# Optimization experiments

Hardware: AMD Instinct MI355X
Metric: run time of the kernel (lower is better)

## Reference

```python
import jax, jax.numpy as jnp
import numpy as np

R, TOTAL, N_NODE, B = 4, 32768, 1024, 32
D_IN, D_HID, C, H, NCLS = 256, 256, 8, 8, 10
E = 262144


def setup_inputs() -> dict:
    key = jax.random.key(0)
    ks = jax.random.split(key, 20)
    s = 0.05  # weight scale for numerical stability
    return {
        "h": jax.random.normal(ks[0], (TOTAL, D_IN), jnp.float32),
        "src": jax.random.randint(ks[1], (R, E), 0, TOTAL),
        "dst": jax.random.randint(ks[2], (R, E), 0, TOTAL),
        "node_label": jax.random.randint(ks[3], (TOTAL,), 0, C),
        "feat_label": jax.random.randint(ks[4], (D_HID,), 0, C),
        "W1": jax.random.normal(ks[5], (R, D_IN, D_HID), jnp.float32) * s,
        "b1": jnp.zeros((R, D_HID), jnp.float32),
        "W2": jax.random.normal(ks[6], (R, D_HID, D_HID), jnp.float32) * s,
        "b2": jnp.zeros((R, D_HID), jnp.float32),
        "Wr": jax.random.normal(ks[7], (C, D_HID, D_HID), jnp.float32) * s,
        "br": jnp.zeros((C, D_HID), jnp.float32),
        "Wq": jax.random.normal(ks[8], (D_HID, D_HID), jnp.float32) * s,
        "Wk": jax.random.normal(ks[9], (D_HID, D_HID), jnp.float32) * s,
        "Wv": jax.random.normal(ks[10], (D_HID, D_HID), jnp.float32) * s,
        "lin_w": jax.random.normal(ks[11], (D_HID, D_HID), jnp.float32) * s,
        "lin_b": jnp.zeros((D_HID,), jnp.float32),
        "bn_gamma": jnp.ones((D_HID,), jnp.float32),
        "bn_beta": jnp.zeros((D_HID,), jnp.float32),
        "cls_w": jax.random.normal(ks[12], (NCLS, D_HID), jnp.float32) * s,
        "cls_b": jnp.zeros((NCLS,), jnp.float32),
    }


def _gconv(x, src, dst, W, b, n):
    # DGL GraphConv norm='both' with self-loops added (dgl.add_self_loop)
    loop = jnp.arange(n)
    s = jnp.concatenate([src, loop])
    d = jnp.concatenate([dst, loop])
    ones = jnp.ones(s.shape, jnp.float32)
    deg_out = jnp.maximum(jax.ops.segment_sum(ones, s, num_segments=n), 1.0)
    deg_in = jnp.maximum(jax.ops.segment_sum(ones, d, num_segments=n), 1.0)
    msg = x[s] * jax.lax.rsqrt(deg_out)[s][:, None]          # [E+n, D]
    agg = jax.ops.segment_sum(msg, d, num_segments=n)        # [n, D]
    agg = agg * jax.lax.rsqrt(deg_in)[:, None]
    return agg @ W + b


def _hetero_layer(x, src, dst, W, b, n):
    # HeteroGraphConv: per-relation GraphConv, 'sum' cross-relation aggregation
    out = 0.0
    for r in range(R):
        out = out + _gconv(x, src[r], dst[r], W[r], b[r], n)
    return out


def _attention(x, Wq, Wk, Wv, lin_w, lin_b):
    # FeatureAttentionLayer (eval mode: no attn dropout)
    b, c, d = x.shape
    dh = d // H
    q = (x @ Wq).reshape(b, c, H, dh).transpose(2, 0, 1, 3)   # [H,B,C,dh]
    k = (x @ Wk).reshape(b, c, H, dh).transpose(2, 0, 1, 3)
    v = (x @ Wv).reshape(b, c, H, dh).transpose(2, 0, 1, 3)
    scores = jnp.einsum('hbqd,hbkd->hbqk', q, k) / jnp.sqrt(jnp.float32(c))
    attn = jax.nn.softmax(scores, axis=-1)
    o = jnp.einsum('hbqk,hbkd->hbqd', attn, v)
    o = o.transpose(1, 2, 0, 3).reshape(b, c, d)              # [B,C,D]
    ff = jax.nn.relu(o @ lin_w.T + lin_b) + o                 # feedforward + inner residual
    out = ff + x                                              # outer residual
    return jnp.mean(out, axis=1)                              # [B,D]


def reference(h, src, dst, node_label, feat_label, W1, b1, W2, b2, Wr, br,
              Wq, Wk, Wv, lin_w, lin_b, bn_gamma, bn_beta, cls_w, cls_b):
    n = h.shape[0]
    # RGCN: conv1 -> relu -> conv2
    h1 = jax.nn.relu(_hetero_layer(h, src, dst, W1, b1, n))
    h2 = _hetero_layer(h1, src, dst, W2, b2, n)               # [TOTAL, D_HID]

    node_emb = h2.reshape(B, N_NODE, D_HID)
    node_mask0 = node_label.reshape(B, N_NODE)[0]             # first graph's node types

    # cluster-wise masked pooling + per-cluster linear resize
    pooled = []
    for key in range(C):
        fmask = (feat_label == key).astype(h2.dtype)          # [D]
        nmask = (node_mask0 == key).astype(h2.dtype)          # [N]
        cnt = jnp.maximum(nmask.sum(), 1.0)
        v = jnp.einsum('bnd,n->bd', node_emb, nmask) / cnt    # mean over cluster's nodes
        v = v * fmask[None, :]                                # keep only cluster's features
        pooled.append(v @ Wr[key].T + br[key])
    emb_in = jnp.stack(pooled, axis=1)                        # [B, C, D]

    graph_emb = _attention(emb_in, Wq, Wk, Wv, lin_w, lin_b)  # [B, D]

    hg_raw = jnp.mean(node_emb, axis=1)                       # dgl.mean_nodes per graph
    diff = graph_emb.reshape(-1) - hg_raw.reshape(-1)
    recon = jnp.sqrt(jnp.sum(jnp.square(diff + 1e-6)))        # pairwise_distance p=2

    # BatchNorm1d with batch statistics, dropout identity (eval)
    mu = jnp.mean(graph_emb, axis=0)
    var = jnp.var(graph_emb, axis=0)
    hg = (graph_emb - mu) * jax.lax.rsqrt(var + 1e-5) * bn_gamma + bn_beta
    logits = hg @ cls_w.T + cls_b                             # [B, NCLS]
    return logits, recon
```

## Files before the change

kernel.cpp:

```cpp
#include <hip/hip_runtime.h>
#include <math.h>

#define R_ 4
#define TOTAL_ 32768
#define NNODE_ 1024
#define B_ 32
#define DH_ 256
#define C_ 8
#define H_ 8
#define NCLS_ 10
#define E_ 262144
#define S_ 32
#define CHUNK_ (E_ / S_)

typedef __attribute__((ext_vector_type(4))) float f32x4;
typedef __attribute__((ext_vector_type(2))) float f32x2;
typedef __attribute__((ext_vector_type(2))) unsigned int uint2v;
typedef __attribute__((ext_vector_type(4))) unsigned int uint4v;
typedef long long i64;

__device__ inline unsigned short f2bf(float f) {
  unsigned int u = __builtin_bit_cast(unsigned int, f);
  u += 0x7FFF + ((u >> 16) & 1);
  return (unsigned short)(u >> 16);
}
__device__ inline float bf2f(unsigned short s) {
  return __builtin_bit_cast(float, (unsigned int)s << 16);
}


__global__ __launch_bounds__(1024) void hist_part(const int* __restrict__ src,
                                                  const int* __restrict__ dst,
                                                  unsigned int* __restrict__ parts) {
  int r = blockIdx.y, s = blockIdx.x, t = threadIdx.x;
  __shared__ unsigned int hs[16384], hd[16384];
  for (int i = t; i < 16384; i += 1024) { hs[i] = 0; hd[i] = 0; }
  __syncthreads();
  const int* sp = src + (size_t)r * E_ + s * CHUNK_;
  const int* dp = dst + (size_t)r * E_ + s * CHUNK_;
  for (int i = t; i < CHUNK_; i += 1024) {
    int a = sp[i], b = dp[i];
    atomicAdd(&hs[a >> 1], 1u << ((a & 1) * 16));
    atomicAdd(&hd[b >> 1], 1u << ((b & 1) * 16));
  }
  __syncthreads();
  unsigned int* po = parts + ((size_t)(r * S_ + s) * 2) * 16384;
  for (int i = t; i < 16384; i += 1024) { po[i] = hs[i]; po[16384 + i] = hd[i]; }
}

__global__ void reduce_deg(const unsigned int* __restrict__ parts,
                           float* __restrict__ rs_out, float* __restrict__ rs_in,
                           int* __restrict__ cnt_in) {
  int gid = blockIdx.x * 256 + threadIdx.x;
  int r = gid >> 14, w = gid & 16383;
  unsigned int s0 = 0, s1 = 0, d0 = 0, d1 = 0;
  for (int s = 0; s < S_; s++) {
    unsigned int ws_ = parts[((size_t)(r * S_ + s) * 2) * 16384 + w];
    unsigned int wd  = parts[((size_t)(r * S_ + s) * 2 + 1) * 16384 + w];
    s0 += ws_ & 0xffff; s1 += ws_ >> 16;
    d0 += wd & 0xffff;  d1 += wd >> 16;
  }
  int n0 = w * 2, n1 = n0 + 1;
  rs_out[r * TOTAL_ + n0] = rsqrtf((float)(s0 + 1));
  rs_out[r * TOTAL_ + n1] = rsqrtf((float)(s1 + 1));
  rs_in[r * TOTAL_ + n0]  = rsqrtf((float)(d0 + 1));
  rs_in[r * TOTAL_ + n1]  = rsqrtf((float)(d1 + 1));
  cnt_in[r * TOTAL_ + n0] = (int)d0;
  cnt_in[r * TOTAL_ + n1] = (int)d1;
}

__global__ __launch_bounds__(1024) void scan_counts(const int* __restrict__ cnt_in,
                                                    int* __restrict__ off) {
  int r = blockIdx.x;
  const int* c = cnt_in + r * TOTAL_;
  int* o = off + r * (TOTAL_ + 1);
  __shared__ int part[1024];
  int t = threadIdx.x;
  int base = t * 32;
  int loc[32];
  int s = 0;
#pragma unroll
  for (int j = 0; j < 32; j++) { loc[j] = c[base + j]; s += loc[j]; }
  part[t] = s;
  __syncthreads();
  for (int d = 1; d < 1024; d <<= 1) {
    int v = (t >= d) ? part[t - d] : 0;
    __syncthreads();
    part[t] += v;
    __syncthreads();
  }
  int run = (t == 0) ? 0 : part[t - 1];
#pragma unroll
  for (int j = 0; j < 32; j++) {
    o[base + j] = run;
    run += loc[j];
  }
  if (t == 1023) o[TOTAL_] = run;
}

__global__ void base_gen(const unsigned int* __restrict__ parts,
                         const int* __restrict__ csr_off,
                         unsigned int* __restrict__ sbb) {
  int gid = blockIdx.x * 256 + threadIdx.x;
  int r = gid >> 14, w = gid & 16383;
  int n0 = w * 2, n1 = n0 + 1;
  unsigned int run0 = (unsigned int)csr_off[r * (TOTAL_ + 1) + n0];
  unsigned int run1 = (unsigned int)csr_off[r * (TOTAL_ + 1) + n1];
  for (int s = 0; s < S_; s++) {
    unsigned int wd = parts[((size_t)(r * S_ + s) * 2 + 1) * 16384 + w];
    sbb[(size_t)(r * S_ + s) * TOTAL_ + n0] = run0;
    sbb[(size_t)(r * S_ + s) * TOTAL_ + n1] = run1;
    run0 += wd & 0xffff;
    run1 += wd >> 16;
  }
}

__global__ __launch_bounds__(1024) void scatter_csr(const int* __restrict__ src,
                                                    const int* __restrict__ dst,
                                                    const unsigned int* __restrict__ sbb,
                                                    int* __restrict__ csr_src) {
  int r = blockIdx.y, s = blockIdx.x, t = threadIdx.x;
  __shared__ unsigned int basel[TOTAL_];
  const unsigned int* sb = sbb + (size_t)(r * S_ + s) * TOTAL_;
  for (int i = t; i < TOTAL_; i += 1024) basel[i] = sb[i];
  __syncthreads();
  const int* sp = src + (size_t)r * E_ + s * CHUNK_;
  const int* dp = dst + (size_t)r * E_ + s * CHUNK_;
  int* co = csr_src + (size_t)r * E_;
  for (int i = t; i < CHUNK_; i += 1024) {
    int d = dp[i];
    unsigned int slot = atomicAdd(&basel[d], 1u);
    co[slot] = sp[i];
  }
}


__global__ void hconv8(const float* __restrict__ x, unsigned int* __restrict__ xq) {
  size_t i = (size_t)blockIdx.x * blockDim.x + threadIdx.x;
  float4 a = ((const float4*)x)[2 * i];
  float4 b = ((const float4*)x)[2 * i + 1];
  unsigned int lo = 0, hi = 0;
  lo = __builtin_amdgcn_cvt_pk_fp8_f32(a.x, a.y, lo, false);
  lo = __builtin_amdgcn_cvt_pk_fp8_f32(a.z, a.w, lo, true);
  hi = __builtin_amdgcn_cvt_pk_fp8_f32(b.x, b.y, hi, false);
  hi = __builtin_amdgcn_cvt_pk_fp8_f32(b.z, b.w, hi, true);
  uint2v o; o[0] = lo; o[1] = hi;
  *(uint2v*)&xq[2 * i] = o;
}

__global__ void wconv_f8(const float* __restrict__ W1, const float* __restrict__ W2,
                         unsigned int* __restrict__ T1, unsigned int* __restrict__ T2) {
  int id = blockIdx.x * blockDim.x + threadIdx.x;
  const float* W = (id < 65536) ? W1 : W2;
  unsigned int* T = (id < 65536) ? T1 : T2;
  int j = id & 65535;
  int c = j >> 8, kq = j & 255;
  int k0 = kq * 4;
  float w0 = W[(size_t)(k0 + 0) * 256 + c];
  float w1 = W[(size_t)(k0 + 1) * 256 + c];
  float w2 = W[(size_t)(k0 + 2) * 256 + c];
  float w3 = W[(size_t)(k0 + 3) * 256 + c];
  unsigned int o = 0;
  o = __builtin_amdgcn_cvt_pk_fp8_f32(w0, w1, o, false);
  o = __builtin_amdgcn_cvt_pk_fp8_f32(w2, w3, o, true);
  T[(size_t)c * 256 + kq] = o;
}

__global__ void bias_sum2(const float* __restrict__ b1, const float* __restrict__ b2,
                          float* __restrict__ s1, float* __restrict__ s2) {
  const float* b = blockIdx.x ? b2 : b1;
  float* s = blockIdx.x ? s2 : s1;
  int d = threadIdx.x;
  s[d] = b[d] + b[DH_ + d] + b[2 * DH_ + d] + b[3 * DH_ + d];
}

__global__ void transpose_mats(const float* __restrict__ Wr, const float* __restrict__ lw,
                               float* __restrict__ Wrt, float* __restrict__ lwt) {
  int i = blockIdx.x * blockDim.x + threadIdx.x;
  int m = i >> 16, j = i & 65535;
  int row = j >> 8, col = j & 255;
  float v = (m < 8) ? Wr[(size_t)m * 65536 + j] : lw[j];
  float* T = (m < 8) ? (Wrt + (size_t)m * 65536) : lwt;
  T[col * 256 + row] = v;
}

__global__ __launch_bounds__(256) void aggregate_f8(
    const unsigned int* __restrict__ xq, const int* __restrict__ csr_off,
    const int* __restrict__ csr_src, const float* __restrict__ rs_out,
    const float* __restrict__ rs_in, unsigned int* __restrict__ aggQ) {
  int r = blockIdx.y;
  int node = blockIdx.x * 8 + (threadIdx.x >> 5);
  int lane5 = threadIdx.x & 31;
  const int* offr = csr_off + r * (TOTAL_ + 1);
  const int* srcs = csr_src + (size_t)r * E_;
  const float* rso = rs_out + r * TOTAL_;
  float a0, a1, a2, a3, a4, a5, a6, a7;
  {
    uint2v v = *(const uint2v*)&xq[(size_t)node * 64 + lane5 * 2];
    float w = rso[node];
    f32x2 p;
    p = __builtin_amdgcn_cvt_pk_f32_fp8(v[0], false); a0 = p[0] * w; a1 = p[1] * w;
    p = __builtin_amdgcn_cvt_pk_f32_fp8(v[0], true);  a2 = p[0] * w; a3 = p[1] * w;
    p = __builtin_amdgcn_cvt_pk_f32_fp8(v[1], false); a4 = p[0] * w; a5 = p[1] * w;
    p = __builtin_amdgcn_cvt_pk_f32_fp8(v[1], true);  a6 = p[0] * w; a7 = p[1] * w;
  }
  int e0 = offr[node], e1 = offr[node + 1];
  int e = e0;
  for (; e + 4 <= e1; e += 4) {
    int s0 = srcs[e], s1 = srcs[e + 1], s2 = srcs[e + 2], s3 = srcs[e + 3];
    uint2v v0 = *(const uint2v*)&xq[(size_t)s0 * 64 + lane5 * 2];
    uint2v v1 = *(const uint2v*)&xq[(size_t)s1 * 64 + lane5 * 2];
    uint2v v2 = *(const uint2v*)&xq[(size_t)s2 * 64 + lane5 * 2];
    uint2v v3 = *(const uint2v*)&xq[(size_t)s3 * 64 + lane5 * 2];
    float w0 = rso[s0], w1 = rso[s1], w2 = rso[s2], w3 = rso[s3];
    f32x2 p;
    p = __builtin_amdgcn_cvt_pk_f32_fp8(v0[0], false); a0 += p[0] * w0; a1 += p[1] * w0;
    p = __builtin_amdgcn_cvt_pk_f32_fp8(v0[0], true);  a2 += p[0] * w0; a3 += p[1] * w0;
    p = __builtin_amdgcn_cvt_pk_f32_fp8(v0[1], false); a4 += p[0] * w0; a5 += p[1] * w0;
    p = __builtin_amdgcn_cvt_pk_f32_fp8(v0[1], true);  a6 += p[0] * w0; a7 += p[1] * w0;
    p = __builtin_amdgcn_cvt_pk_f32_fp8(v1[0], false); a0 += p[0] * w1; a1 += p[1] * w1;
    p = __builtin_amdgcn_cvt_pk_f32_fp8(v1[0], true);  a2 += p[0] * w1; a3 += p[1] * w1;
    p = __builtin_amdgcn_cvt_pk_f32_fp8(v1[1], false); a4 += p[0] * w1; a5 += p[1] * w1;
    p = __builtin_amdgcn_cvt_pk_f32_fp8(v1[1], true);  a6 += p[0] * w1; a7 += p[1] * w1;
    p = __builtin_amdgcn_cvt_pk_f32_fp8(v2[0], false); a0 += p[0] * w2; a1 += p[1] * w2;
    p = __builtin_amdgcn_cvt_pk_f32_fp8(v2[0], true);  a2 += p[0] * w2; a3 += p[1] * w2;
    p = __builtin_amdgcn_cvt_pk_f32_fp8(v2[1], false); a4 += p[0] * w2; a5 += p[1] * w2;
    p = __builtin_amdgcn_cvt_pk_f32_fp8(v2[1], true);  a6 += p[0] * w2; a7 += p[1] * w2;
    p = __builtin_amdgcn_cvt_pk_f32_fp8(v3[0], false); a0 += p[0] * w3; a1 += p[1] * w3;
    p = __builtin_amdgcn_cvt_pk_f32_fp8(v3[0], true);  a2 += p[0] * w3; a3 += p[1] * w3;
    p = __builtin_amdgcn_cvt_pk_f32_fp8(v3[1], false); a4 += p[0] * w3; a5 += p[1] * w3;
    p = __builtin_amdgcn_cvt_pk_f32_fp8(v3[1], true);  a6 += p[0] * w3; a7 += p[1] * w3;
  }
  for (; e < e1; e++) {
    int s0 = srcs[e];
    uint2v v0 = *(const uint2v*)&xq[(size_t)s0 * 64 + lane5 * 2];
    float w0 = rso[s0];
    f32x2 p;
    p = __builtin_amdgcn_cvt_pk_f32_fp8(v0[0], false); a0 += p[0] * w0; a1 += p[1] * w0;
    p = __builtin_amdgcn_cvt_pk_f32_fp8(v0[0], true);  a2 += p[0] * w0; a3 += p[1] * w0;
    p = __builtin_amdgcn_cvt_pk_f32_fp8(v0[1], false); a4 += p[0] * w0; a5 += p[1] * w0;
    p = __builtin_amdgcn_cvt_pk_f32_fp8(v0[1], true);  a6 += p[0] * w0; a7 += p[1] * w0;
  }
  float wi = rs_in[r * TOTAL_ + node];
  unsigned int o0 = 0, o1 = 0;
  o0 = __builtin_amdgcn_cvt_pk_fp8_f32(a0 * wi, a1 * wi, o0, false);
  o0 = __builtin_amdgcn_cvt_pk_fp8_f32(a2 * wi, a3 * wi, o0, true);
  o1 = __builtin_amdgcn_cvt_pk_fp8_f32(a4 * wi, a5 * wi, o1, false);
  o1 = __builtin_amdgcn_cvt_pk_fp8_f32(a6 * wi, a7 * wi, o1, true);
  uint2v o; o[0] = o0; o[1] = o1;
  *(uint2v*)&aggQ[(size_t)node * 256 + r * 64 + lane5 * 2] = o;
}

template <int MODE>
__global__ __launch_bounds__(256) void gemm_f8(
    const unsigned char* __restrict__ A, const unsigned char* __restrict__ Bt,
    const float* __restrict__ bias, unsigned char* __restrict__ out8,
    unsigned short* __restrict__ out16) {
  __shared__ unsigned char As[128][80];
  __shared__ unsigned char Bs[128][80];
  int t = threadIdx.x;
  int row0 = blockIdx.x * 128, col0 = blockIdx.y * 128;
  int wid = t >> 6, lane = t & 63;
  int wm = wid >> 1, wn = wid & 1;
  int lr = lane & 15, lk = lane >> 4;
  f32x4 acc[4][4] = {};
  for (int k0 = 0; k0 < 1024; k0 += 64) {
#pragma unroll
    for (int i = 0; i < 2; i++) {
      int c = t + 256 * i;
      int rr = c >> 2, cc = (c & 3) * 16;
      *(uint4v*)&As[rr][cc] = *(const uint4v*)&A[(size_t)(row0 + rr) * 1024 + k0 + cc];
      *(uint4v*)&Bs[rr][cc] = *(const uint4v*)&Bt[(size_t)(col0 + rr) * 1024 + k0 + cc];
    }
    __syncthreads();
#pragma unroll
    for (int kk = 0; kk < 2; kk++) {
      i64 afr[4], bfr[4];
#pragma unroll
      for (int m = 0; m < 4; m++) afr[m] = *(const i64*)&As[wm * 64 + m * 16 + lr][kk * 32 + lk * 8];
#pragma unroll
      for (int n = 0; n < 4; n++) bfr[n] = *(const i64*)&Bs[wn * 64 + n * 16 + lr][kk * 32 + lk * 8];
#pragma unroll
      for (int m = 0; m < 4; m++)
#pragma unroll
        for (int n = 0; n < 4; n++)
          acc[m][n] = __builtin_amdgcn_mfma_f32_16x16x32_fp8_fp8(afr[m], bfr[n], acc[m][n], 0, 0, 0);
    }
    __syncthreads();
  }
  int lq = lane >> 4;
#pragma unroll
  for (int m = 0; m < 4; m++) {
    int row = row0 + wm * 64 + m * 16 + lq * 4;
#pragma unroll
    for (int n = 0; n < 4; n++) {
      int col = col0 + wn * 64 + n * 16 + lr;
      float bv = bias[col];
#pragma unroll
      for (int q = 0; q < 4; q++) {
        float v = acc[m][n][q] + bv;
        if (MODE == 0) {
          v = fmaxf(v, 0.f);
          int b8 = __builtin_amdgcn_cvt_pk_fp8_f32(v, 0.f, 0, false);
          out8[(size_t)(row + q) * DH_ + col] = (unsigned char)b8;
        } else {
          out16[(size_t)(row + q) * DH_ + col] = f2bf(v);
        }
      }
    }
  }
}


__global__ __launch_bounds__(256) void pool_part(const unsigned short* __restrict__ h2b,
                                                 const int* __restrict__ node_label,
                                                 float* __restrict__ part) {
  int b = blockIdx.x, ch = blockIdx.y, d = threadIdx.x;
  __shared__ int slab[128];
  if (d < 128) slab[d] = node_label[ch * 128 + d];
  __syncthreads();
  float a[C_] = {0.f};
  float at = 0.f;
  const unsigned short* base = h2b + ((size_t)b * NNODE_ + ch * 128) * DH_ + d;
  for (int n = 0; n < 128; n++) {
    float x = bf2f(base[(size_t)n * DH_]);
    int lab = slab[n];
    at += x;
#pragma unroll
    for (int k = 0; k < C_; k++) a[k] += (lab == k) ? x : 0.f;
  }
  float* pb = part + ((size_t)(ch * B_ + b) * 9) * DH_ + d;
#pragma unroll
  for (int k = 0; k < C_; k++) pb[(size_t)k * DH_] = a[k];
  pb[(size_t)8 * DH_] = at;
}

__global__ __launch_bounds__(256) void pool_fin(const float* __restrict__ part,
                                                const int* __restrict__ node_label,
                                                const int* __restrict__ feat_label,
                                                float* __restrict__ poolv,
                                                float* __restrict__ hg_raw) {
  int b = blockIdx.x, d = threadIdx.x;
  __shared__ int cnt[C_];
  if (d < C_) cnt[d] = 0;
  __syncthreads();
  for (int n = d; n < NNODE_; n += 256) atomicAdd(&cnt[node_label[n]], 1);
  __syncthreads();
  float s[9];
#pragma unroll
  for (int k = 0; k < 9; k++) s[k] = 0.f;
  for (int ch = 0; ch < 8; ch++) {
    const float* pb = part + ((size_t)(ch * B_ + b) * 9) * DH_ + d;
#pragma unroll
    for (int k = 0; k < 9; k++) s[k] += pb[(size_t)k * DH_];
  }
  int fl = feat_label[d];
#pragma unroll
  for (int k = 0; k < C_; k++) {
    float cntf = fmaxf((float)cnt[k], 1.f);
    float v = (fl == k) ? (s[k] / cntf) : 0.f;
    poolv[((size_t)k * B_ + b) * DH_ + d] = v;
  }
  hg_raw[(size_t)b * DH_ + d] = s[8] * (1.f / NNODE_);
}


__global__ __launch_bounds__(256) void rq_t(const float* __restrict__ poolv,
                                            const float* __restrict__ Wrt,
                                            const float* __restrict__ br,
                                            const float* __restrict__ Wq,
                                            const float* __restrict__ Wk,
                                            const float* __restrict__ Wv,
                                            float* __restrict__ emb,
                                            float* __restrict__ q, float* __restrict__ k,
                                            float* __restrict__ v) {
  int key = blockIdx.x & 7, b = blockIdx.x >> 3, t = threadIdx.x;
  __shared__ float pl[DH_], es[DH_];
  pl[t] = poolv[((size_t)key * B_ + b) * DH_ + t];
  __syncthreads();
  const float* W = Wrt + (size_t)key * DH_ * DH_;
  float s = 0.f;
  for (int d = 0; d < DH_; d++) s += pl[d] * W[d * DH_ + t];
  s += br[key * DH_ + t];
  es[t] = s;
  size_t idx = (size_t)b * C_ + key;
  emb[idx * DH_ + t] = s;
  __syncthreads();
  float sq = 0.f, sk = 0.f, sv = 0.f;
  for (int kk = 0; kk < DH_; kk++) {
    float xv = es[kk];
    sq += xv * Wq[kk * DH_ + t];
    sk += xv * Wk[kk * DH_ + t];
    sv += xv * Wv[kk * DH_ + t];
  }
  q[idx * DH_ + t] = sq;
  k[idx * DH_ + t] = sk;
  v[idx * DH_ + t] = sv;
}

__global__ __launch_bounds__(256) void attn_core(const float* __restrict__ q,
                                                 const float* __restrict__ k,
                                                 const float* __restrict__ v,
                                                 float* __restrict__ osb) {
  int b = blockIdx.x, t = threadIdx.x;
  __shared__ float qs[C_][DH_], ks[C_][DH_], vs[C_][DH_];
  __shared__ float sc[H_][C_][C_];
  for (int c = 0; c < C_; c++) {
    qs[c][t] = q[((size_t)b * C_ + c) * DH_ + t];
    ks[c][t] = k[((size_t)b * C_ + c) * DH_ + t];
    vs[c][t] = v[((size_t)b * C_ + c) * DH_ + t];
  }
  __syncthreads();
  for (int idx = t; idx < H_ * C_ * C_; idx += 256) {
    int hh = idx / (C_ * C_);
    int qc = (idx / C_) % C_;
    int kc = idx % C_;
    float s = 0.f;
    for (int dd = 0; dd < 32; dd++) s += qs[qc][hh * 32 + dd] * ks[kc][hh * 32 + dd];
    sc[hh][qc][kc] = s * 0.35355339059327373f;
  }
  __syncthreads();
  if (t < H_ * C_) {
    int hh = t / C_, qc = t % C_;
    float m = -1e30f;
    for (int kc = 0; kc < C_; kc++) m = fmaxf(m, sc[hh][qc][kc]);
    float sum = 0.f;
    for (int kc = 0; kc < C_; kc++) { float e = expf(sc[hh][qc][kc] - m); sc[hh][qc][kc] = e; sum += e; }
    float inv = 1.f / sum;
    for (int kc = 0; kc < C_; kc++) sc[hh][qc][kc] *= inv;
  }
  __syncthreads();
  int hh = t >> 5;
  for (int c = 0; c < C_; c++) {
    float s = 0.f;
#pragma unroll
    for (int kc = 0; kc < C_; kc++) s += sc[hh][c][kc] * vs[kc][t];
    osb[((size_t)b * C_ + c) * DH_ + t] = s;
  }
}

__global__ __launch_bounds__(256) void ff_res(const float* __restrict__ osb,
                                              const float* __restrict__ emb,
                                              const float* __restrict__ lwt,
                                              const float* __restrict__ lb,
                                              float* __restrict__ ffb) {
  int idx = blockIdx.x, t = threadIdx.x;
  __shared__ float ox[DH_];
  ox[t] = osb[(size_t)idx * DH_ + t];
  __syncthreads();
  float s = 0.f;
  for (int d = 0; d < DH_; d++) s += ox[d] * lwt[d * DH_ + t];
  ffb[(size_t)idx * DH_ + t] =
      fmaxf(s + lb[t], 0.f) + ox[t] + emb[(size_t)idx * DH_ + t];
}

__global__ __launch_bounds__(256) void tail_final(
    const float* __restrict__ ffb, const float* __restrict__ hg_raw,
    const float* __restrict__ g, const float* __restrict__ be,
    const float* __restrict__ cw, const float* __restrict__ cb,
    float* __restrict__ out) {
  int t = threadIdx.x;
  __shared__ float hgn[B_][DH_];
  __shared__ float red[256];
  float gcol[B_];
  float mu = 0.f;
#pragma unroll
  for (int b = 0; b < B_; b++) {
    float s = 0.f;
    for (int c = 0; c < C_; c++) s += ffb[((size_t)b * C_ + c) * DH_ + t];
    gcol[b] = s * (1.f / C_);
    mu += gcol[b];
  }
  mu *= (1.f / B_);
  float var = 0.f;
#pragma unroll
  for (int b = 0; b < B_; b++) { float x = gcol[b] - mu; var += x * x; }
  var *= (1.f / B_);
  float is = rsqrtf(var + 1e-5f);
  float gm = g[t], bt = be[t];
  float s = 0.f;
#pragma unroll
  for (int b = 0; b < B_; b++) {
    hgn[b][t] = (gcol[b] - mu) * is * gm + bt;
    float d = gcol[b] - hg_raw[b * DH_ + t] + 1e-6f;
    s += d * d;
  }
  red[t] = s;
  __syncthreads();
  for (int w = 128; w > 0; w >>= 1) {
    if (t < w) red[t] += red[t + w];
    __syncthreads();
  }
  if (t == 0) out[B_ * NCLS_] = sqrtf(red[0]);
  for (int o = t; o < B_ * NCLS_; o += 256) {
    int b = o / NCLS_, j = o % NCLS_;
    float sl = cb[j];
    for (int d = 0; d < DH_; d++) sl += hgn[b][d] * cw[j * DH_ + d];
    out[o] = sl;
  }
}


extern "C" void kernel_launch(void* const* d_in, const int* in_sizes, int n_in,
                              void* d_out, int out_size, void* d_ws, size_t ws_size,
                              hipStream_t stream) {
  const float* h   = (const float*)d_in[0];
  const int* src   = (const int*)d_in[1];
  const int* dst   = (const int*)d_in[2];
  const int* nlab  = (const int*)d_in[3];
  const int* flab  = (const int*)d_in[4];
  const float* W1  = (const float*)d_in[5];
  const float* b1  = (const float*)d_in[6];
  const float* W2  = (const float*)d_in[7];
  const float* b2  = (const float*)d_in[8];
  const float* Wr  = (const float*)d_in[9];
  const float* br  = (const float*)d_in[10];
  const float* Wq  = (const float*)d_in[11];
  const float* Wk  = (const float*)d_in[12];
  const float* Wv  = (const float*)d_in[13];
  const float* lw  = (const float*)d_in[14];
  const float* lb  = (const float*)d_in[15];
  const float* bng = (const float*)d_in[16];
  const float* bnb = (const float*)d_in[17];
  const float* cw  = (const float*)d_in[18];
  const float* cb  = (const float*)d_in[19];
  float* out = (float*)d_out;

  char* p = (char*)d_ws;
  auto alloc = [&](size_t bytes) -> void* {
    void* q = (void*)p;
    p += (bytes + 255) & ~(size_t)255;
    return q;
  };
  unsigned int* xq    = (unsigned int*)alloc((size_t)TOTAL_ * DH_);
  unsigned int* h1q   = (unsigned int*)alloc((size_t)TOTAL_ * DH_);
  unsigned short* h2b = (unsigned short*)alloc((size_t)TOTAL_ * DH_ * 2);
  unsigned int* aggQ  = (unsigned int*)alloc((size_t)TOTAL_ * 1024);
  unsigned int* Wq1   = (unsigned int*)alloc((size_t)256 * 256 * 4);
  unsigned int* Wq2   = (unsigned int*)alloc((size_t)256 * 256 * 4);
  float* Wrt   = (float*)alloc((size_t)C_ * DH_ * DH_ * 4);
  float* lwt   = (float*)alloc((size_t)DH_ * DH_ * 4);
  float* bsum1 = (float*)alloc(DH_ * 4);
  float* bsum2 = (float*)alloc(DH_ * 4);
  int* cnt_in   = (int*)alloc((size_t)R_ * TOTAL_ * 4);
  float* rs_out = (float*)alloc((size_t)R_ * TOTAL_ * 4);
  float* rs_in  = (float*)alloc((size_t)R_ * TOTAL_ * 4);
  int* csr_off  = (int*)alloc((size_t)R_ * (TOTAL_ + 1) * 4);
  int* csr_src  = (int*)alloc((size_t)R_ * E_ * 4);
  float* part   = (float*)alloc((size_t)8 * B_ * 9 * DH_ * 4);
  float* poolv  = (float*)alloc((size_t)C_ * B_ * DH_ * 4);
  float* hg_raw = (float*)alloc((size_t)B_ * DH_ * 4);
  float* emb    = (float*)alloc((size_t)B_ * C_ * DH_ * 4);
  float* qb     = (float*)alloc((size_t)B_ * C_ * DH_ * 4);
  float* kb     = (float*)alloc((size_t)B_ * C_ * DH_ * 4);
  float* vb     = (float*)alloc((size_t)B_ * C_ * DH_ * 4);
  float* osb    = (float*)alloc((size_t)B_ * C_ * DH_ * 4);
  float* ffb    = (float*)alloc((size_t)B_ * C_ * DH_ * 4);

  unsigned int* parts = aggQ;
  unsigned int* sbb   = (unsigned int*)((char*)aggQ + (size_t)16 * 1024 * 1024);

  hist_part<<<dim3(S_, R_), 1024, 0, stream>>>(src, dst, parts);
  reduce_deg<<<R_ * TOTAL_ / 512, 256, 0, stream>>>(parts, rs_out, rs_in, cnt_in);
  scan_counts<<<R_, 1024, 0, stream>>>(cnt_in, csr_off);
  base_gen<<<R_ * TOTAL_ / 512, 256, 0, stream>>>(parts, csr_off, sbb);
  scatter_csr<<<dim3(S_, R_), 1024, 0, stream>>>(src, dst, sbb, csr_src);

  wconv_f8<<<512, 256, 0, stream>>>(W1, W2, Wq1, Wq2);
  bias_sum2<<<2, 256, 0, stream>>>(b1, b2, bsum1, bsum2);
  transpose_mats<<<9 * 256, 256, 0, stream>>>(Wr, lw, Wrt, lwt);
  hconv8<<<TOTAL_ * DH_ / 8 / 256, 256, 0, stream>>>(h, xq);

  aggregate_f8<<<dim3(TOTAL_ / 8, R_), 256, 0, stream>>>(xq, csr_off, csr_src, rs_out, rs_in, aggQ);
  gemm_f8<0><<<dim3(TOTAL_ / 128, 2), 256, 0, stream>>>(
      (const unsigned char*)aggQ, (const unsigned char*)Wq1, bsum1,
      (unsigned char*)h1q, nullptr);

  aggregate_f8<<<dim3(TOTAL_ / 8, R_), 256, 0, stream>>>(h1q, csr_off, csr_src, rs_out, rs_in, aggQ);
  gemm_f8<1><<<dim3(TOTAL_ / 128, 2), 256, 0, stream>>>(
      (const unsigned char*)aggQ, (const unsigned char*)Wq2, bsum2,
      nullptr, h2b);

  pool_part<<<dim3(B_, 8), 256, 0, stream>>>(h2b, nlab, part);
  pool_fin<<<B_, 256, 0, stream>>>(part, nlab, flab, poolv, hg_raw);
  rq_t<<<B_ * C_, 256, 0, stream>>>(poolv, Wrt, br, Wq, Wk, Wv, emb, qb, kb, vb);
  attn_core<<<B_, 256, 0, stream>>>(qb, kb, vb, osb);
  ff_res<<<B_ * C_, 256, 0, stream>>>(osb, emb, lwt, lb, ffb);
  tail_final<<<1, 256, 0, stream>>>(ffb, hg_raw, bng, bnb, cw, cb, out);
}
```

Baseline: 300.4 us.

## Split histogram and CSR scatter across more blocks; fuse attention with feed-forward

The histogram kernel now processes src and dst in separate blocks, each with a single 64KB shared array, which doubles the grid and should raise occupancy. The CSR scatter splits the destination range into two halves so each block keeps only a 64KB base table in LDS, at the cost of every block reading the full dst chunk and skipping half the edges. The attention core and feed-forward residual kernels are merged, so the attention output stays in shared memory and each weight load is reused across 8 clusters. The fused kernel runs only 32 blocks instead of 256, which may hurt latency on the linear layer.

```diff
diff --git a/kernel.cpp b/kernel.cpp
--- a/kernel.cpp
+++ b/kernel.cpp
@@ -32,20 +32,18 @@
 __global__ __launch_bounds__(1024) void hist_part(const int* __restrict__ src,
                                                   const int* __restrict__ dst,
                                                   unsigned int* __restrict__ parts) {
-  int r = blockIdx.y, s = blockIdx.x, t = threadIdx.x;
-  __shared__ unsigned int hs[16384], hd[16384];
-  for (int i = t; i < 16384; i += 1024) { hs[i] = 0; hd[i] = 0; }
-  __syncthreads();
-  const int* sp = src + (size_t)r * E_ + s * CHUNK_;
-  const int* dp = dst + (size_t)r * E_ + s * CHUNK_;
+  int r = blockIdx.y, s = blockIdx.x, which = blockIdx.z, t = threadIdx.x;
+  __shared__ unsigned int hh[16384];
+  for (int i = t; i < 16384; i += 1024) hh[i] = 0;
+  __syncthreads();
+  const int* ep = (which ? dst : src) + (size_t)r * E_ + s * CHUNK_;
   for (int i = t; i < CHUNK_; i += 1024) {
-    int a = sp[i], b = dp[i];
-    atomicAdd(&hs[a >> 1], 1u << ((a & 1) * 16));
-    atomicAdd(&hd[b >> 1], 1u << ((b & 1) * 16));
-  }
-  __syncthreads();
-  unsigned int* po = parts + ((size_t)(r * S_ + s) * 2) * 16384;
-  for (int i = t; i < 16384; i += 1024) { po[i] = hs[i]; po[16384 + i] = hd[i]; }
+    int a = ep[i];
+    atomicAdd(&hh[a >> 1], 1u << ((a & 1) * 16));
+  }
+  __syncthreads();
+  unsigned int* po = parts + ((size_t)(r * S_ + s) * 2 + which) * 16384;
+  for (int i = t; i < 16384; i += 1024) po[i] = hh[i];
 }
 
 __global__ void reduce_deg(const unsigned int* __restrict__ parts,
@@ -119,18 +117,20 @@
                                                     const int* __restrict__ dst,
                                                     const unsigned int* __restrict__ sbb,
                                                     int* __restrict__ csr_src) {
-  int r = blockIdx.y, s = blockIdx.x, t = threadIdx.x;
-  __shared__ unsigned int basel[TOTAL_];
-  const unsigned int* sb = sbb + (size_t)(r * S_ + s) * TOTAL_;
-  for (int i = t; i < TOTAL_; i += 1024) basel[i] = sb[i];
+  int r = blockIdx.y, s = blockIdx.x, half = blockIdx.z, t = threadIdx.x;
+  __shared__ unsigned int basel[16384];
+  const unsigned int* sb = sbb + (size_t)(r * S_ + s) * TOTAL_ + half * 16384;
+  for (int i = t; i < 16384; i += 1024) basel[i] = sb[i];
   __syncthreads();
   const int* sp = src + (size_t)r * E_ + s * CHUNK_;
   const int* dp = dst + (size_t)r * E_ + s * CHUNK_;
   int* co = csr_src + (size_t)r * E_;
   for (int i = t; i < CHUNK_; i += 1024) {
     int d = dp[i];
-    unsigned int slot = atomicAdd(&basel[d], 1u);
-    co[slot] = sp[i];
+    if ((d >> 14) == half) {
+      unsigned int slot = atomicAdd(&basel[d & 16383], 1u);
+      co[slot] = sp[i];
+    }
   }
 }
 
@@ -398,12 +398,15 @@
   v[idx * DH_ + t] = sv;
 }
 
-__global__ __launch_bounds__(256) void attn_core(const float* __restrict__ q,
-                                                 const float* __restrict__ k,
-                                                 const float* __restrict__ v,
-                                                 float* __restrict__ osb) {
+__global__ __launch_bounds__(256) void attn_ff(const float* __restrict__ q,
+                                               const float* __restrict__ k,
+                                               const float* __restrict__ v,
+                                               const float* __restrict__ emb,
+                                               const float* __restrict__ lwt,
+                                               const float* __restrict__ lb,
+                                               float* __restrict__ ffb) {
   int b = blockIdx.x, t = threadIdx.x;
-  __shared__ float qs[C_][DH_], ks[C_][DH_], vs[C_][DH_];
+  __shared__ float qs[C_][DH_], ks[C_][DH_], vs[C_][DH_], os[C_][DH_];
   __shared__ float sc[H_][C_][C_];
   for (int c = 0; c < C_; c++) {
     qs[c][t] = q[((size_t)b * C_ + c) * DH_ + t];
@@ -435,23 +438,21 @@
     float s = 0.f;
 #pragma unroll
     for (int kc = 0; kc < C_; kc++) s += sc[hh][c][kc] * vs[kc][t];
-    osb[((size_t)b * C_ + c) * DH_ + t] = s;
-  }
-}
-
-__global__ __launch_bounds__(256) void ff_res(const float* __restrict__ osb,
-                                              const float* __restrict__ emb,
-                                              const float* __restrict__ lwt,
-                                              const float* __restrict__ lb,
-                                              float* __restrict__ ffb) {
-  int idx = blockIdx.x, t = threadIdx.x;
-  __shared__ float ox[DH_];
-  ox[t] = osb[(size_t)idx * DH_ + t];
-  __syncthreads();
-  float s = 0.f;
-  for (int d = 0; d < DH_; d++) s += ox[d] * lwt[d * DH_ + t];
-  ffb[(size_t)idx * DH_ + t] =
-      fmaxf(s + lb[t], 0.f) + ox[t] + emb[(size_t)idx * DH_ + t];
+    os[c][t] = s;
+  }
+  __syncthreads();
+  float s[C_] = {0.f};
+  for (int d = 0; d < DH_; d++) {
+    float w = lwt[d * DH_ + t];
+#pragma unroll
+    for (int c = 0; c < C_; c++) s[c] += os[c][d] * w;
+  }
+  float lbv = lb[t];
+#pragma unroll
+  for (int c = 0; c < C_; c++) {
+    ffb[((size_t)b * C_ + c) * DH_ + t] =
+        fmaxf(s[c] + lbv, 0.f) + os[c][t] + emb[((size_t)b * C_ + c) * DH_ + t];
+  }
 }
 
 __global__ __launch_bounds__(256) void tail_final(
@@ -554,17 +555,16 @@
   float* qb     = (float*)alloc((size_t)B_ * C_ * DH_ * 4);
   float* kb     = (float*)alloc((size_t)B_ * C_ * DH_ * 4);
   float* vb     = (float*)alloc((size_t)B_ * C_ * DH_ * 4);
-  float* osb    = (float*)alloc((size_t)B_ * C_ * DH_ * 4);
   float* ffb    = (float*)alloc((size_t)B_ * C_ * DH_ * 4);
 
   unsigned int* parts = aggQ;
   unsigned int* sbb   = (unsigned int*)((char*)aggQ + (size_t)16 * 1024 * 1024);
 
-  hist_part<<<dim3(S_, R_), 1024, 0, stream>>>(src, dst, parts);
+  hist_part<<<dim3(S_, R_, 2), 1024, 0, stream>>>(src, dst, parts);
   reduce_deg<<<R_ * TOTAL_ / 512, 256, 0, stream>>>(parts, rs_out, rs_in, cnt_in);
   scan_counts<<<R_, 1024, 0, stream>>>(cnt_in, csr_off);
   base_gen<<<R_ * TOTAL_ / 512, 256, 0, stream>>>(parts, csr_off, sbb);
-  scatter_csr<<<dim3(S_, R_), 1024, 0, stream>>>(src, dst, sbb, csr_src);
+  scatter_csr<<<dim3(S_, R_, 2), 1024, 0, stream>>>(src, dst, sbb, csr_src);
 
   wconv_f8<<<512, 256, 0, stream>>>(W1, W2, Wq1, Wq2);
   bias_sum2<<<2, 256, 0, stream>>>(b1, b2, bsum1, bsum2);
@@ -584,7 +584,6 @@
   pool_part<<<dim3(B_, 8), 256, 0, stream>>>(h2b, nlab, part);
   pool_fin<<<B_, 256, 0, stream>>>(part, nlab, flab, poolv, hg_raw);
   rq_t<<<B_ * C_, 256, 0, stream>>>(poolv, Wrt, br, Wq, Wk, Wv, emb, qb, kb, vb);
-  attn_core<<<B_, 256, 0, stream>>>(qb, kb, vb, osb);
-  ff_res<<<B_ * C_, 256, 0, stream>>>(osb, emb, lwt, lb, ffb);
+  attn_ff<<<B_, 256, 0, stream>>>(qb, kb, vb, emb, lwt, lb, ffb);
   tail_final<<<1, 256, 0, stream>>>(ffb, hg_raw, bng, bnb, cw, cb, out);
 }
```

Result: slower. 306.9 us (+2.2%).
